# Performance work log

Measured on AMD Instinct MI355X. Metric: run time of the kernel, lower is better.

## Reference

```python
import jax, jax.numpy as jnp
import numpy as np

B, SEQ_LEN, PRED_LEN, LABEL_LEN, PERIOD, N_CH = 32, 2048, 1024, 512, 256, 256
K = SEQ_LEN // PERIOD   # seg_num_x = 8
L = PRED_LEN // PERIOD  # seg_num_y = 4
EPS = 1e-5


def setup_inputs() -> dict:
    key = jax.random.key(0)
    k1, k2, k3, k4, k5, k6, k7 = jax.random.split(key, 7)
    x_enc = jax.random.normal(k1, (B, SEQ_LEN, N_CH), jnp.float32)
    x_mark_enc = jax.random.normal(k2, (B, SEQ_LEN, 4), jnp.float32)
    x_dec = jax.random.normal(k3, (B, LABEL_LEN + PRED_LEN, N_CH), jnp.float32)
    x_mark_dec = jax.random.normal(k4, (B, LABEL_LEN + PRED_LEN, 4), jnp.float32)
    # base_model abstracted as a linear map on the time axis of a [B, PERIOD, N] segment.
    # Scaled ~1/sqrt(P) so repeated powers (up to K+L-1 = 11) stay numerically tame.
    W_base = jax.random.normal(k5, (PERIOD, PERIOD), jnp.float32) * (0.9 / np.sqrt(PERIOD))
    # new_encoders[j]: nn.Linear(seg_num_x, 1) -> weight row [K] + bias scalar per j.
    W_enc = jax.random.normal(k6, (L, K), jnp.float32) * (1.0 / np.sqrt(K))
    b_enc = jax.random.normal(k7, (L,), jnp.float32) * 0.01
    return {"x_enc": x_enc, "x_mark_enc": x_mark_enc, "x_dec": x_dec,
            "x_mark_dec": x_mark_dec, "W_base": W_base, "W_enc": W_enc, "b_enc": b_enc}


def reference(x_enc, x_mark_enc, x_dec, x_mark_dec, W_base, W_enc, b_enc):
    Bv, S, N = x_enc.shape
    # per-series normalization over time (means is .detach()'d in torch; fwd math identical)
    means = jnp.mean(x_enc, axis=1, keepdims=True)                  # [B,1,N]
    xc = x_enc - means
    stdev = jnp.sqrt(jnp.var(xc, axis=1, keepdims=True) + EPS)      # [B,1,N]
    xn = xc / stdev

    # split into K segments of length PERIOD: [K, B, P, N]
    segs = xn.reshape(Bv, K, PERIOD, N).transpose(1, 0, 2, 3)

    # x_res[l][k] = base_model applied (K - k + l) times to segment k.
    # base(x) = einsum('qp,bpn->bqn', W_base, x), so m applications = W_base^m.
    def step(c, _):
        nxt = W_base @ c
        return nxt, nxt
    _, rest = jax.lax.scan(step, W_base, None, length=K + L - 2)
    powers = jnp.concatenate([W_base[None], rest], axis=0)          # powers[i] = W^(i+1)

    exps = (K - jnp.arange(K))[None, :] + jnp.arange(L)[:, None]    # [L,K]
    Wlk = powers[exps - 1]                                          # [L,K,P,P]
    x_res = jnp.einsum('lkqp,kbpn->lkbqn', Wlk, segs)               # [L,K,B,P,N]

    # dec_out_part[l] = sum_k W_enc[l,k] * x_res[l][k] + b_enc[l] * ones
    dec = jnp.einsum('lk,lkbqn->lbqn', W_enc, x_res) + b_enc[:, None, None, None]
    dec = dec.transpose(1, 0, 2, 3).reshape(Bv, L * PERIOD, N)      # cat over time

    # de-normalize
    dec = dec * stdev[:, 0, :][:, None, :] + means[:, 0, :][:, None, :]
    return dec[:, -PRED_LEN:, :]
```

## Files before the change

### kernel.cpp

```cpp
#include <hip/hip_runtime.h>
#include <cstdint>
#include <cstddef>


typedef unsigned short ushort_t;
typedef unsigned int uint_t;
typedef __attribute__((ext_vector_type(8))) short bf16x8;
typedef __attribute__((ext_vector_type(16))) float f32x16;

__device__ __forceinline__ ushort_t f32_to_bf16(float f) {
    uint_t u = __float_as_uint(f);
    u += 0x7FFFu + ((u >> 16) & 1u);
    return (ushort_t)(u >> 16);
}
__device__ __forceinline__ float bf16_to_f32(ushort_t h) {
    return __uint_as_float((uint_t)h << 16);
}

struct PowOps { int sa[4]; int sb[4]; int sd[4]; };

__global__ void powmul(const float* __restrict__ Wb, float* __restrict__ Pw, PowOps ops) {
    __shared__ float As[4 * 256];
    const int mat = blockIdx.x;
    const int r0  = blockIdx.y * 4;
    const int tid = threadIdx.x;
    const float* A  = (ops.sa[mat] < 0) ? Wb : Pw + (size_t)ops.sa[mat] * 65536;
    const float* Bm = (ops.sb[mat] < 0) ? Wb : Pw + (size_t)ops.sb[mat] * 65536;
    float* C        = Pw + (size_t)ops.sd[mat] * 65536;
#pragma unroll
    for (int i = 0; i < 4; ++i) As[i * 256 + tid] = A[(size_t)(r0 + i) * 256 + tid];
    __syncthreads();
    float a0 = 0.f, a1 = 0.f, a2 = 0.f, a3 = 0.f;
    for (int p = 0; p < 256; p += 8) {
        float bv[8];
#pragma unroll
        for (int u = 0; u < 8; ++u) bv[u] = Bm[(size_t)(p + u) * 256 + tid];
#pragma unroll
        for (int u = 0; u < 8; ++u) {
            a0 += As[0 * 256 + p + u] * bv[u];
            a1 += As[1 * 256 + p + u] * bv[u];
            a2 += As[2 * 256 + p + u] * bv[u];
            a3 += As[3 * 256 + p + u] * bv[u];
        }
    }
    C[(size_t)(r0 + 0) * 256 + tid] = a0;
    C[(size_t)(r0 + 1) * 256 + tid] = a1;
    C[(size_t)(r0 + 2) * 256 + tid] = a2;
    C[(size_t)(r0 + 3) * 256 + tid] = a3;
}

__global__ void prepPb(const float* __restrict__ Pw, const float* __restrict__ Wb,
                       ushort_t* __restrict__ Pb, float* __restrict__ prs) {
    const int ib = blockIdx.x;
    const int e  = ib >> 2;
    const int rq = ib & 3;
    const int tid = threadIdx.x;
    const int q  = rq * 64 + (tid >> 2);
    const int cc = tid & 3;
    uint2* dst = (uint2*)(Pb + (size_t)e * 65536 + q * 256 + cc * 64);
    float s = 0.f;
    if (e == 0) {
#pragma unroll
        for (int i = 0; i < 16; ++i) {
            uint2 o; o.x = 0u; o.y = 0u;
            const int col0 = cc * 64 + i * 4;
            if (q >= col0 && q < col0 + 4) {
                const int j = q - col0;
                if (j == 0) o.x = 0x3F80u; else if (j == 1) o.x = 0x3F800000u;
                else if (j == 2) o.y = 0x3F80u; else o.y = 0x3F800000u;
            }
            dst[i] = o;
        }
        s = 1.0f;
    } else {
        const float* src = (e == 1) ? Wb : (Pw + (size_t)(e - 2) * 65536);
        const float4* sp = (const float4*)(src + (size_t)q * 256 + cc * 64);
#pragma unroll
        for (int i = 0; i < 16; ++i) {
            const float4 v = sp[i];
            const ushort_t h0 = f32_to_bf16(v.x), h1 = f32_to_bf16(v.y);
            const ushort_t h2 = f32_to_bf16(v.z), h3 = f32_to_bf16(v.w);
            s += bf16_to_f32(h0) + bf16_to_f32(h1) + bf16_to_f32(h2) + bf16_to_f32(h3);
            uint2 o; o.x = (uint_t)h0 | ((uint_t)h1 << 16); o.y = (uint_t)h2 | ((uint_t)h3 << 16);
            dst[i] = o;
        }
    }
    s += __shfl_xor(s, 1);
    s += __shfl_xor(s, 2);
    if (cc == 0) prs[e * 256 + q] = s;
}

#define GLOAD_LDS16(gsrc, ldst) \
    __builtin_amdgcn_global_load_lds((const __attribute__((address_space(1))) void*)(gsrc), \
                                     (__attribute__((address_space(3))) void*)(ldst), 16, 0, 0)

__global__ __launch_bounds__(512, 4) void gemm_v(
    const ushort_t* __restrict__ Pb, const float* __restrict__ x,
    ushort_t* __restrict__ vt,
    float* __restrict__ psS1, float* __restrict__ psS2)
{
    __shared__ ushort_t sA[2][4096];
    __shared__ ushort_t sB[3][8192];
    __shared__ uint_t   scr[32 * 64];

    const int bid  = blockIdx.x;
    const int k    = bid & 7;
    const int colT = bid >> 3;
    const int e    = 8 - k;

    const int tid  = threadIdx.x;
    const int lane = tid & 63;
    const int w    = tid >> 6;
    const int wm   = w >> 2;
    const int wq   = w & 3;
    const int li   = lane & 31, lg = lane >> 5;
    const int lq3  = (li >> 1) & 3;
    const int lrow = 2 * (lane >> 3) + ((lane >> 2) & 1);
    const int kc   = (lane & 3) ^ ((lane >> 3) & 3);

    const ushort_t* pbb = Pb + (size_t)e * 65536;
    const int b  = colT >> 1;
    const int n0 = (colT & 1) * 128;
    const float* xseg = x + ((size_t)b * 2048 + k * 256) * 256 + n0;

    const int xp = tid >> 5;
    const int xn = (tid & 31) * 4;

    float4 xr[2];
    float s1[4] = {0, 0, 0, 0}, s2[4] = {0, 0, 0, 0};

#define BSTAGE(bf_, kt_) do { \
    const int p0_ = (kt_) * 32 + kc * 8; \
    GLOAD_LDS16(pbb + (w * 32 + 0  + lrow) * 256 + p0_, &sB[bf_][(w * 32 + 0)  * 32]); \
    GLOAD_LDS16(pbb + (w * 32 + 16 + lrow) * 256 + p0_, &sB[bf_][(w * 32 + 16) * 32]); \
} while (0)

#define XLOAD(kt_) do { \
    xr[0] = *(const float4*)(xseg + (size_t)((kt_) * 32 + xp)      * 256 + xn); \
    xr[1] = *(const float4*)(xseg + (size_t)((kt_) * 32 + xp + 16) * 256 + xn); \
} while (0)

#define SCRW() do { \
    _Pragma("unroll") \
    for (int i_ = 0; i_ < 2; ++i_) { \
        const float4 v_ = xr[i_]; \
        s1[0] += v_.x; s2[0] += v_.x * v_.x; \
        s1[1] += v_.y; s2[1] += v_.y * v_.y; \
        s1[2] += v_.z; s2[2] += v_.z * v_.z; \
        s1[3] += v_.w; s2[3] += v_.w * v_.w; \
        uint2 p_; \
        p_.x = (uint_t)f32_to_bf16(v_.x) | ((uint_t)f32_to_bf16(v_.y) << 16); \
        p_.y = (uint_t)f32_to_bf16(v_.z) | ((uint_t)f32_to_bf16(v_.w) << 16); \
        *(uint2*)(scr + (xp + 16 * i_) * 64 + (xn >> 1)) = p_; \
    } \
} while (0)

#define FRAGBUILD(buf_) do { \
    const int R_ = tid >> 2;                  \
    const int pc_ = tid & 3;                  \
    const int sh_ = (R_ & 1) * 16; \
    uint_t o_[4]; \
    _Pragma("unroll") \
    for (int u_ = 0; u_ < 4; ++u_) { \
        const uint_t w0_ = scr[(pc_ * 8 + 2 * u_ + 0) * 64 + (R_ >> 1)]; \
        const uint_t w1_ = scr[(pc_ * 8 + 2 * u_ + 1) * 64 + (R_ >> 1)]; \
        o_[u_] = ((w0_ >> sh_) & 0xFFFFu) | (((w1_ >> sh_) & 0xFFFFu) << 16); \
    } \
    uint4 q_; q_.x = o_[0]; q_.y = o_[1]; q_.z = o_[2]; q_.w = o_[3]; \
    *(uint4*)((char*)&sA[buf_][0] + R_ * 64 + ((pc_ ^ ((R_ >> 1) & 3)) << 4)) = q_; \
} while (0)

    f32x16 acc[2][2];
#pragma unroll
    for (int mm = 0; mm < 2; ++mm)
#pragma unroll
        for (int nn = 0; nn < 2; ++nn)
#pragma unroll
            for (int rr = 0; rr < 16; ++rr) acc[mm][nn][rr] = 0.0f;

    XLOAD(0);
    asm volatile("s_waitcnt vmcnt(0)" ::: "memory");
    SCRW();
    asm volatile("s_waitcnt lgkmcnt(0)" ::: "memory");
    __builtin_amdgcn_s_barrier();
    asm volatile("" ::: "memory");
    FRAGBUILD(0);
    BSTAGE(0, 0);
    asm volatile("" ::: "memory");
    XLOAD(1);
    asm volatile("" ::: "memory");
    BSTAGE(1, 1);
    asm volatile("s_waitcnt lgkmcnt(0)" ::: "memory");

#define VKT(kt_) do { \
    if ((kt_) < 7) { asm volatile("s_waitcnt vmcnt(2)" ::: "memory"); } \
    else           { asm volatile("s_waitcnt vmcnt(0)" ::: "memory"); } \
    __builtin_amdgcn_s_barrier(); \
    asm volatile("" ::: "memory"); \
    const ushort_t* pa_ = &sA[(kt_) & 1][0]; \
    const ushort_t* px_ = &sB[(kt_) % 3][0]; \
    bf16x8 af0, af1, xf0, xf1; \
    { const int sl_ = lg ^ lq3; \
      const int ro_ = (li >> 1) * 64 + (li & 1) * 32 + sl_ * 8; \
      af0 = *(const bf16x8*)(pa_ + wm * 2048 + ro_); \
      af1 = *(const bf16x8*)(pa_ + wm * 2048 + 1024 + ro_); \
      xf0 = *(const bf16x8*)(px_ + wq * 2048 + ro_); \
      xf1 = *(const bf16x8*)(px_ + wq * 2048 + 1024 + ro_); } \
    if ((kt_) < 7) { SCRW(); }    \
    if ((kt_) < 6) { \
        XLOAD((kt_) + 2); \
        asm volatile("" ::: "memory"); \
        BSTAGE(((kt_) + 2) % 3, (kt_) + 2); \
    } \
    __builtin_amdgcn_s_setprio(1); \
    acc[0][0] = __builtin_amdgcn_mfma_f32_32x32x16_bf16(af0, xf0, acc[0][0], 0, 0, 0); \
    acc[0][1] = __builtin_amdgcn_mfma_f32_32x32x16_bf16(af0, xf1, acc[0][1], 0, 0, 0); \
    acc[1][0] = __builtin_amdgcn_mfma_f32_32x32x16_bf16(af1, xf0, acc[1][0], 0, 0, 0); \
    acc[1][1] = __builtin_amdgcn_mfma_f32_32x32x16_bf16(af1, xf1, acc[1][1], 0, 0, 0); \
    { const int sl_ = (2 + lg) ^ lq3; \
      const int ro_ = (li >> 1) * 64 + (li & 1) * 32 + sl_ * 8; \
      af0 = *(const bf16x8*)(pa_ + wm * 2048 + ro_); \
      af1 = *(const bf16x8*)(pa_ + wm * 2048 + 1024 + ro_); \
      xf0 = *(const bf16x8*)(px_ + wq * 2048 + ro_); \
      xf1 = *(const bf16x8*)(px_ + wq * 2048 + 1024 + ro_); } \
    acc[0][0] = __builtin_amdgcn_mfma_f32_32x32x16_bf16(af0, xf0, acc[0][0], 0, 0, 0); \
    acc[0][1] = __builtin_amdgcn_mfma_f32_32x32x16_bf16(af0, xf1, acc[0][1], 0, 0, 0); \
    acc[1][0] = __builtin_amdgcn_mfma_f32_32x32x16_bf16(af1, xf0, acc[1][0], 0, 0, 0); \
    acc[1][1] = __builtin_amdgcn_mfma_f32_32x32x16_bf16(af1, xf1, acc[1][1], 0, 0, 0); \
    __builtin_amdgcn_s_setprio(0); \
    asm volatile("" ::: "memory"); \
    if ((kt_) < 7) { \
        asm volatile("s_waitcnt lgkmcnt(0)" ::: "memory"); \
        __builtin_amdgcn_s_barrier(); \
        asm volatile("" ::: "memory"); \
        FRAGBUILD(((kt_) + 1) & 1); \
        asm volatile("s_waitcnt lgkmcnt(0)" ::: "memory"); \
    } \
} while (0)

    VKT(0); VKT(1); VKT(2); VKT(3); VKT(4); VKT(5); VKT(6); VKT(7);
#undef VKT
#undef FRAGBUILD
#undef SCRW
#undef XLOAD
#undef BSTAGE

    ushort_t* vb = vt + (size_t)k * 2097152;
#pragma unroll
    for (int mm = 0; mm < 2; ++mm)
#pragma unroll
        for (int nn = 0; nn < 2; ++nn) {
            const int q = wq * 64 + nn * 32 + li;
#pragma unroll
            for (int rr = 0; rr < 16; ++rr) {
                const int c = colT * 128 + wm * 64 + mm * 32 + ((rr & 3) + 8 * (rr >> 2) + 4 * lg);
                vb[(size_t)c * 256 + q] = f32_to_bf16(acc[mm][nn][rr]);
            }
        }

    __syncthreads();
    float* sf = (float*)&sB[0][0];
    *(float4*)(sf + xp * 128 + xn)        = make_float4(s1[0], s1[1], s1[2], s1[3]);
    *(float4*)(sf + 2048 + xp * 128 + xn) = make_float4(s2[0], s2[1], s2[2], s2[3]);
    __syncthreads();
    if (tid < 128) {
        float a = 0.f;
#pragma unroll
        for (int r = 0; r < 16; ++r) a += sf[r * 128 + tid];
        psS1[(size_t)k * 8192 + colT * 128 + tid] = a;
    } else if (tid < 256) {
        const int tt = tid - 128;
        float a = 0.f;
#pragma unroll
        for (int r = 0; r < 16; ++r) a += sf[2048 + r * 128 + tt];
        psS2[(size_t)k * 8192 + colT * 128 + tt] = a;
    }
}

__global__ void combine(const ushort_t* __restrict__ vt, const float* __restrict__ Wenc,
                        ushort_t* __restrict__ c,
                        const float* __restrict__ psS1, const float* __restrict__ psS2,
                        const float* __restrict__ prs, const ushort_t* __restrict__ Pb,
                        float* __restrict__ meanv, float* __restrict__ stdv,
                        float* __restrict__ rsA) {
    __shared__ float uf[256];
    const int bid = blockIdx.x;
    const int t   = threadIdx.x;
    if (bid < 1024) {
        const int col = bid * 8 + (t >> 5);
        const size_t off = (size_t)col * 256 + (t & 31) * 8;
        float a0[8] = {0,0,0,0,0,0,0,0}, a1[8] = {0,0,0,0,0,0,0,0};
        float a2[8] = {0,0,0,0,0,0,0,0}, a3[8] = {0,0,0,0,0,0,0,0};
#pragma unroll
        for (int k = 0; k < 8; ++k) {
            const bf16x8 v = *(const bf16x8*)(vt + (size_t)k * 2097152 + off);
            const float w0 = Wenc[0 * 8 + k], w1 = Wenc[1 * 8 + k];
            const float w2 = Wenc[2 * 8 + k], w3 = Wenc[3 * 8 + k];
#pragma unroll
            for (int j = 0; j < 8; ++j) {
                const float f = bf16_to_f32((ushort_t)v[j]);
                a0[j] += w0 * f; a1[j] += w1 * f; a2[j] += w2 * f; a3[j] += w3 * f;
            }
        }
        bf16x8 o0, o1, o2, o3;
#pragma unroll
        for (int j = 0; j < 8; ++j) {
            o0[j] = (short)f32_to_bf16(a0[j]); o1[j] = (short)f32_to_bf16(a1[j]);
            o2[j] = (short)f32_to_bf16(a2[j]); o3[j] = (short)f32_to_bf16(a3[j]);
        }
        *(bf16x8*)(c + 0 * 2097152 + off) = o0;
        *(bf16x8*)(c + 1 * 2097152 + off) = o1;
        *(bf16x8*)(c + 2 * 2097152 + off) = o2;
        *(bf16x8*)(c + 3 * 2097152 + off) = o3;
    } else if (bid < 1056) {
        const int b = bid - 1024;
        const int col = b * 256 + t;
        float s = 0.f, q = 0.f;
#pragma unroll
        for (int k = 0; k < 8; ++k) {
            s += psS1[(size_t)k * 8192 + col];
            q += psS2[(size_t)k * 8192 + col];
        }
        const float mean = s * (1.0f / 2048.0f);
        float var = q * (1.0f / 2048.0f) - mean * mean;
        var = fmaxf(var, 0.0f);
        meanv[col] = mean;
        stdv [col] = sqrtf(var + 1e-5f);
    } else {
        const int l = bid - 1056;
        float u = 0.f;
#pragma unroll
        for (int k = 0; k < 8; ++k) u += Wenc[l * 8 + k] * prs[(8 - k) * 256 + t];
        uf[t] = u;
        __syncthreads();
        const uint2* rp = (const uint2*)(Pb + (size_t)l * 65536 + t * 256);
        float s = 0.f;
#pragma unroll
        for (int i = 0; i < 64; ++i) {
            const uint2 v = rp[i];
            s += bf16_to_f32((ushort_t)(v.x & 0xffff)) * uf[i * 4 + 0]
               + bf16_to_f32((ushort_t)(v.x >> 16))    * uf[i * 4 + 1]
               + bf16_to_f32((ushort_t)(v.y & 0xffff)) * uf[i * 4 + 2]
               + bf16_to_f32((ushort_t)(v.y >> 16))    * uf[i * 4 + 3];
        }
        rsA[l * 256 + t] = s;
    }
}

__global__ __launch_bounds__(256, 2) void gemm2(
    const ushort_t* __restrict__ Pb, const ushort_t* __restrict__ c,
    const float* __restrict__ meanv, const float* __restrict__ stdv,
    const float* __restrict__ rsA, const float* __restrict__ benc,
    float* __restrict__ out)
{
    __shared__ ushort_t sAa[3][4096];
    __shared__ ushort_t sBb[3][4096];

    const int bid  = blockIdx.x;
    const int xcd  = bid & 7;
    const int g    = bid >> 3;
    const int colT = xcd + ((g & 7) << 3);
    const int rest = g >> 3;
    const int l    = rest >> 1;
    const int qpT  = rest & 1;

    const int tid  = threadIdx.x;
    const int lane = tid & 63;
    const int w    = tid >> 6;
    const int wm   = w >> 1, wn = w & 1;
    const int li   = lane & 31, lg = lane >> 5;
    const int lq3  = (li >> 1) & 3;
    const int lrow = 2 * (lane >> 3) + ((lane >> 2) & 1);
    const int kc   = (lane & 3) ^ ((lane >> 3) & 3);

    const ushort_t* ab = Pb + (size_t)l * 65536 + (size_t)(qpT * 128) * 256;
    const ushort_t* cb = c + ((size_t)l * 8192 + colT * 128) * 256;

#define GSTAGE(bf_, kt_) do { \
    const int p0_ = (kt_) * 32 + kc * 8; \
    GLOAD_LDS16(ab + (w * 32 + 0  + lrow) * 256 + p0_, &sAa[bf_][(w * 32 + 0)  * 32]); \
    GLOAD_LDS16(ab + (w * 32 + 16 + lrow) * 256 + p0_, &sAa[bf_][(w * 32 + 16) * 32]); \
    GLOAD_LDS16(cb + (w * 32 + 0  + lrow) * 256 + p0_, &sBb[bf_][(w * 32 + 0)  * 32]); \
    GLOAD_LDS16(cb + (w * 32 + 16 + lrow) * 256 + p0_, &sBb[bf_][(w * 32 + 16) * 32]); \
} while (0)

    f32x16 acc[2][2];
#pragma unroll
    for (int mm = 0; mm < 2; ++mm)
#pragma unroll
        for (int nn = 0; nn < 2; ++nn)
#pragma unroll
            for (int rr = 0; rr < 16; ++rr) acc[mm][nn][rr] = 0.0f;

    GSTAGE(0, 0);
    GSTAGE(1, 1);

#define GKT(kt_) do { \
    if ((kt_) < 7) { asm volatile("s_waitcnt vmcnt(4)" ::: "memory"); } \
    else           { asm volatile("s_waitcnt vmcnt(0)" ::: "memory"); } \
    __builtin_amdgcn_s_barrier(); \
    asm volatile("" ::: "memory"); \
    const ushort_t* pa_ = &sAa[(kt_) % 3][0]; \
    const ushort_t* px_ = &sBb[(kt_) % 3][0]; \
    bf16x8 af[2][2], xf[2][2]; \
    _Pragma("unroll") \
    for (int ks = 0; ks < 2; ++ks) { \
        const int sl = ((ks << 1) + lg) ^ lq3; \
        const int ro = (li >> 1) * 64 + (li & 1) * 32 + sl * 8; \
        af[ks][0] = *(const bf16x8*)(pa_ + wm * 2048 + ro); \
        af[ks][1] = *(const bf16x8*)(pa_ + wm * 2048 + 1024 + ro); \
        xf[ks][0] = *(const bf16x8*)(px_ + wn * 2048 + ro); \
        xf[ks][1] = *(const bf16x8*)(px_ + wn * 2048 + 1024 + ro); \
    } \
    if ((kt_) < 6) { GSTAGE(((kt_) + 2) % 3, (kt_) + 2); } \
    __builtin_amdgcn_s_setprio(1); \
    _Pragma("unroll") \
    for (int ks = 0; ks < 2; ++ks) { \
        acc[0][0] = __builtin_amdgcn_mfma_f32_32x32x16_bf16(af[ks][0], xf[ks][0], acc[0][0], 0, 0, 0); \
        acc[0][1] = __builtin_amdgcn_mfma_f32_32x32x16_bf16(af[ks][0], xf[ks][1], acc[0][1], 0, 0, 0); \
        acc[1][0] = __builtin_amdgcn_mfma_f32_32x32x16_bf16(af[ks][1], xf[ks][0], acc[1][0], 0, 0, 0); \
        acc[1][1] = __builtin_amdgcn_mfma_f32_32x32x16_bf16(af[ks][1], xf[ks][1], acc[1][1], 0, 0, 0); \
    } \
    __builtin_amdgcn_s_setprio(0); \
    asm volatile("" ::: "memory"); \
} while (0)

    GKT(0); GKT(1); GKT(2); GKT(3); GKT(4); GKT(5); GKT(6); GKT(7);
#undef GKT
#undef GSTAGE

    const float be = benc[l];
    float mn[2], sd[2];
#pragma unroll
    for (int nn = 0; nn < 2; ++nn) {
        const int col = colT * 128 + wn * 64 + nn * 32 + li;
        mn[nn] = meanv[col];
        sd[nn] = stdv [col];
    }
#pragma unroll
    for (int mm = 0; mm < 2; ++mm)
#pragma unroll
        for (int nn = 0; nn < 2; ++nn) {
            const int col = colT * 128 + wn * 64 + nn * 32 + li;
            const int bq = col >> 8, nq = col & 255;
            const float ben = be * sd[nn];
#pragma unroll
            for (int rr = 0; rr < 16; ++rr) {
                const int trow = l * 256 + qpT * 128 + wm * 64 + mm * 32
                               + ((rr & 3) + 8 * (rr >> 2) + 4 * lg);
                out[((size_t)bq * 1024 + trow) * 256 + nq] =
                    acc[mm][nn][rr] + mn[nn] * (1.0f - rsA[trow]) + ben;
            }
        }
}

extern "C" void kernel_launch(void* const* d_in, const int* in_sizes, int n_in,
                              void* d_out, int out_size, void* d_ws, size_t ws_size,
                              hipStream_t stream) {
    (void)in_sizes; (void)n_in; (void)out_size; (void)ws_size;
    const float* x_enc  = (const float*)d_in[0];
    const float* W_base = (const float*)d_in[4];
    const float* W_enc  = (const float*)d_in[5];
    const float* b_enc  = (const float*)d_in[6];
    float* out = (float*)d_out;

    char* ws = (char*)d_ws;
    float*    wsP    = (float*)(ws);
    ushort_t* wsPb   = (ushort_t*)(ws + 0x200000);
    float*    wsPrs  = (float*)(ws + 0x340000);
    float*    wsS1   = (float*)(ws + 0x350000);
    float*    wsS2   = (float*)(ws + 0x390000);
    float*    wsMean = (float*)(ws + 0x3D0000);
    float*    wsStd  = (float*)(ws + 0x3E0000);
    float*    wsRsA  = (float*)(ws + 0x3F0000);
    ushort_t* wsVt   = (ushort_t*)(ws + 0x400000);
    ushort_t* wsC    = (ushort_t*)(ws + 0x2400000);

    { PowOps o{{-1, 0, 0, 0}, {-1, 0, 0, 0}, {0, 0, 0, 0}};
      powmul<<<dim3(1, 64), 256, 0, stream>>>(W_base, wsP, o); }
    { PowOps o{{0, 0, 0, 0}, {-1, 0, 0, 0}, {1, 2, 0, 0}};
      powmul<<<dim3(2, 64), 256, 0, stream>>>(W_base, wsP, o); }
    { PowOps o{{2, 2, 2, 2}, {-1, 0, 1, 2}, {3, 4, 5, 6}};
      powmul<<<dim3(4, 64), 256, 0, stream>>>(W_base, wsP, o); }

    prepPb<<<36, 256, 0, stream>>>(wsP, W_base, wsPb, wsPrs);

    gemm_v<<<512, 512, 0, stream>>>(wsPb, x_enc, wsVt, wsS1, wsS2);

    combine<<<1060, 256, 0, stream>>>(wsVt, W_enc, wsC, wsS1, wsS2, wsPrs, wsPb,
                                      wsMean, wsStd, wsRsA);

    gemm2<<<512, 256, 0, stream>>>(wsPb, wsC, wsMean, wsStd, wsRsA, b_enc, out);
}
```

Measured before the change: 102.7 us.

## Restructure gemm_v into two halves with batched x staging and padded transpose

The per-k-step pipeline of gemm_v, which interleaved x loads, bf16 transpose and MFMA, becomes two halves. Each half loads 128 rows of x, transposes them into four A-fragment buffers through a scratch area padded to a stride of 65 to avoid LDS bank conflicts, then runs four MFMA k-steps with only one barrier each. The scratch area now aliases the B staging buffers rather than having its own LDS allocation, while the A buffer grows from two slots to four. The aim is fewer barriers and less interleaving overhead in the MFMA loop, at the cost of serialising global x loads ahead of compute in each half and using more LDS in total.

```diff
diff --git a/kernel.cpp b/kernel.cpp
--- a/kernel.cpp
+++ b/kernel.cpp
@@ -99,9 +99,9 @@
     ushort_t* __restrict__ vt,
     float* __restrict__ psS1, float* __restrict__ psS2)
 {
-    __shared__ ushort_t sA[2][4096];
+    __shared__ ushort_t sA[4][4096];
     __shared__ ushort_t sB[3][8192];
-    __shared__ uint_t   scr[32 * 64];
+    uint_t* scr = (uint_t*)&sB[1][0];
 
     const int bid  = blockIdx.x;
     const int k    = bid & 7;
@@ -126,7 +126,7 @@
     const int xp = tid >> 5;
     const int xn = (tid & 31) * 4;
 
-    float4 xr[2];
+    float4 xr0[4], xr1[4];
     float s1[4] = {0, 0, 0, 0}, s2[4] = {0, 0, 0, 0};
 
 #define BSTAGE(bf_, kt_) do { \
@@ -135,39 +135,44 @@
     GLOAD_LDS16(pbb + (w * 32 + 16 + lrow) * 256 + p0_, &sB[bf_][(w * 32 + 16) * 32]); \
 } while (0)
 
-#define XLOAD(kt_) do { \
-    xr[0] = *(const float4*)(xseg + (size_t)((kt_) * 32 + xp)      * 256 + xn); \
-    xr[1] = *(const float4*)(xseg + (size_t)((kt_) * 32 + xp + 16) * 256 + xn); \
-} while (0)
-
-#define SCRW() do { \
+#define XLOADS(dst_, p0_) do { \
     _Pragma("unroll") \
-    for (int i_ = 0; i_ < 2; ++i_) { \
-        const float4 v_ = xr[i_]; \
+    for (int i_ = 0; i_ < 4; ++i_) \
+        dst_[i_] = *(const float4*)(xseg + (size_t)((p0_) + xp + 16 * i_) * 256 + xn); \
+} while (0)
+
+#define SCRW(src_) do { \
+    _Pragma("unroll") \
+    for (int i_ = 0; i_ < 4; ++i_) { \
+        const float4 v_ = src_[i_]; \
         s1[0] += v_.x; s2[0] += v_.x * v_.x; \
         s1[1] += v_.y; s2[1] += v_.y * v_.y; \
         s1[2] += v_.z; s2[2] += v_.z * v_.z; \
         s1[3] += v_.w; s2[3] += v_.w * v_.w; \
-        uint2 p_; \
-        p_.x = (uint_t)f32_to_bf16(v_.x) | ((uint_t)f32_to_bf16(v_.y) << 16); \
-        p_.y = (uint_t)f32_to_bf16(v_.z) | ((uint_t)f32_to_bf16(v_.w) << 16); \
-        *(uint2*)(scr + (xp + 16 * i_) * 64 + (xn >> 1)) = p_; \
+        const int pl_ = xp + 16 * i_; \
+        scr[pl_ * 65 + (xn >> 1)]     = (uint_t)f32_to_bf16(v_.x) | ((uint_t)f32_to_bf16(v_.y) << 16); \
+        scr[pl_ * 65 + (xn >> 1) + 1] = (uint_t)f32_to_bf16(v_.z) | ((uint_t)f32_to_bf16(v_.w) << 16); \
     } \
 } while (0)
 
-#define FRAGBUILD(buf_) do { \
-    const int R_ = tid >> 2;                  \
-    const int pc_ = tid & 3;                  \
+#define FRAGBUILD(s_) do { \
+    const int R_  = tid >> 2;               \
+    const int pc_ = tid & 3; \
+    const int np_ = R_ >> 1; \
     const int sh_ = (R_ & 1) * 16; \
-    uint_t o_[4]; \
     _Pragma("unroll") \
-    for (int u_ = 0; u_ < 4; ++u_) { \
-        const uint_t w0_ = scr[(pc_ * 8 + 2 * u_ + 0) * 64 + (R_ >> 1)]; \
-        const uint_t w1_ = scr[(pc_ * 8 + 2 * u_ + 1) * 64 + (R_ >> 1)]; \
-        o_[u_] = ((w0_ >> sh_) & 0xFFFFu) | (((w1_ >> sh_) & 0xFFFFu) << 16); \
+    for (int kh_ = 0; kh_ < 2; ++kh_) { \
+        uint_t o_[4]; \
+        _Pragma("unroll") \
+        for (int u_ = 0; u_ < 4; ++u_) { \
+            const int m_ = kh_ * 16 + pc_ * 4 + u_; \
+            const uint_t w0_ = scr[(2 * m_) * 65 + np_]; \
+            const uint_t w1_ = scr[(2 * m_ + 1) * 65 + np_]; \
+            o_[u_] = ((w0_ >> sh_) & 0xFFFFu) | (((w1_ >> sh_) & 0xFFFFu) << 16); \
+        } \
+        uint4 q_; q_.x = o_[0]; q_.y = o_[1]; q_.z = o_[2]; q_.w = o_[3]; \
+        *(uint4*)((char*)&sA[0][0] + (2 * (s_) + kh_) * 8192 + R_ * 64 + ((pc_ ^ ((R_ >> 1) & 3)) << 4)) = q_; \
     } \
-    uint4 q_; q_.x = o_[0]; q_.y = o_[1]; q_.z = o_[2]; q_.w = o_[3]; \
-    *(uint4*)((char*)&sA[buf_][0] + R_ * 64 + ((pc_ ^ ((R_ >> 1) & 3)) << 4)) = q_; \
 } while (0)
 
     f32x16 acc[2][2];
@@ -178,71 +183,78 @@
 #pragma unroll
             for (int rr = 0; rr < 16; ++rr) acc[mm][nn][rr] = 0.0f;
 
-    XLOAD(0);
-    asm volatile("s_waitcnt vmcnt(0)" ::: "memory");
-    SCRW();
-    asm volatile("s_waitcnt lgkmcnt(0)" ::: "memory");
-    __builtin_amdgcn_s_barrier();
-    asm volatile("" ::: "memory");
-    FRAGBUILD(0);
-    BSTAGE(0, 0);
-    asm volatile("" ::: "memory");
-    XLOAD(1);
-    asm volatile("" ::: "memory");
-    BSTAGE(1, 1);
-    asm volatile("s_waitcnt lgkmcnt(0)" ::: "memory");
-
-#define VKT(kt_) do { \
-    if ((kt_) < 7) { asm volatile("s_waitcnt vmcnt(2)" ::: "memory"); } \
-    else           { asm volatile("s_waitcnt vmcnt(0)" ::: "memory"); } \
+#define GKT(i_, kt_, STAGEOP, VM) do { \
+    VM; \
     __builtin_amdgcn_s_barrier(); \
     asm volatile("" ::: "memory"); \
-    const ushort_t* pa_ = &sA[(kt_) & 1][0]; \
-    const ushort_t* px_ = &sB[(kt_) % 3][0]; \
-    bf16x8 af0, af1, xf0, xf1; \
+    const ushort_t* pa_ = &sA[i_][0]; \
+    const ushort_t* px_ = &sB[(i_) % 3][0]; \
+    bf16x8 af0, af1, xf0, xf1, ag0, ag1, xg0, xg1; \
     { const int sl_ = lg ^ lq3; \
       const int ro_ = (li >> 1) * 64 + (li & 1) * 32 + sl_ * 8; \
       af0 = *(const bf16x8*)(pa_ + wm * 2048 + ro_); \
       af1 = *(const bf16x8*)(pa_ + wm * 2048 + 1024 + ro_); \
       xf0 = *(const bf16x8*)(px_ + wq * 2048 + ro_); \
       xf1 = *(const bf16x8*)(px_ + wq * 2048 + 1024 + ro_); } \
-    if ((kt_) < 7) { SCRW(); }    \
-    if ((kt_) < 6) { \
-        XLOAD((kt_) + 2); \
-        asm volatile("" ::: "memory"); \
-        BSTAGE(((kt_) + 2) % 3, (kt_) + 2); \
-    } \
+    { const int sl_ = (2 + lg) ^ lq3; \
+      const int ro_ = (li >> 1) * 64 + (li & 1) * 32 + sl_ * 8; \
+      ag0 = *(const bf16x8*)(pa_ + wm * 2048 + ro_); \
+      ag1 = *(const bf16x8*)(pa_ + wm * 2048 + 1024 + ro_); \
+      xg0 = *(const bf16x8*)(px_ + wq * 2048 + ro_); \
+      xg1 = *(const bf16x8*)(px_ + wq * 2048 + 1024 + ro_); } \
+    STAGEOP; \
     __builtin_amdgcn_s_setprio(1); \
     acc[0][0] = __builtin_amdgcn_mfma_f32_32x32x16_bf16(af0, xf0, acc[0][0], 0, 0, 0); \
     acc[0][1] = __builtin_amdgcn_mfma_f32_32x32x16_bf16(af0, xf1, acc[0][1], 0, 0, 0); \
     acc[1][0] = __builtin_amdgcn_mfma_f32_32x32x16_bf16(af1, xf0, acc[1][0], 0, 0, 0); \
     acc[1][1] = __builtin_amdgcn_mfma_f32_32x32x16_bf16(af1, xf1, acc[1][1], 0, 0, 0); \
-    { const int sl_ = (2 + lg) ^ lq3; \
-      const int ro_ = (li >> 1) * 64 + (li & 1) * 32 + sl_ * 8; \
-      af0 = *(const bf16x8*)(pa_ + wm * 2048 + ro_); \
-      af1 = *(const bf16x8*)(pa_ + wm * 2048 + 1024 + ro_); \
-      xf0 = *(const bf16x8*)(px_ + wq * 2048 + ro_); \
-      xf1 = *(const bf16x8*)(px_ + wq * 2048 + 1024 + ro_); } \
-    acc[0][0] = __builtin_amdgcn_mfma_f32_32x32x16_bf16(af0, xf0, acc[0][0], 0, 0, 0); \
-    acc[0][1] = __builtin_amdgcn_mfma_f32_32x32x16_bf16(af0, xf1, acc[0][1], 0, 0, 0); \
-    acc[1][0] = __builtin_amdgcn_mfma_f32_32x32x16_bf16(af1, xf0, acc[1][0], 0, 0, 0); \
-    acc[1][1] = __builtin_amdgcn_mfma_f32_32x32x16_bf16(af1, xf1, acc[1][1], 0, 0, 0); \
+    acc[0][0] = __builtin_amdgcn_mfma_f32_32x32x16_bf16(ag0, xg0, acc[0][0], 0, 0, 0); \
+    acc[0][1] = __builtin_amdgcn_mfma_f32_32x32x16_bf16(ag0, xg1, acc[0][1], 0, 0, 0); \
+    acc[1][0] = __builtin_amdgcn_mfma_f32_32x32x16_bf16(ag1, xg0, acc[1][0], 0, 0, 0); \
+    acc[1][1] = __builtin_amdgcn_mfma_f32_32x32x16_bf16(ag1, xg1, acc[1][1], 0, 0, 0); \
     __builtin_amdgcn_s_setprio(0); \
     asm volatile("" ::: "memory"); \
-    if ((kt_) < 7) { \
-        asm volatile("s_waitcnt lgkmcnt(0)" ::: "memory"); \
-        __builtin_amdgcn_s_barrier(); \
-        asm volatile("" ::: "memory"); \
-        FRAGBUILD(((kt_) + 1) & 1); \
-        asm volatile("s_waitcnt lgkmcnt(0)" ::: "memory"); \
-    } \
-} while (0)
-
-    VKT(0); VKT(1); VKT(2); VKT(3); VKT(4); VKT(5); VKT(6); VKT(7);
-#undef VKT
+} while (0)
+
+#define VMW(n_) asm volatile("s_waitcnt vmcnt(" #n_ ")" ::: "memory")
+#define LGW()   asm volatile("s_waitcnt lgkmcnt(0)" ::: "memory")
+#define BARM()  do { __builtin_amdgcn_s_barrier(); asm volatile("" ::: "memory"); } while (0)
+
+#define HALF(h_) do { \
+    XLOADS(xr0, (h_) * 128);         \
+    XLOADS(xr1, (h_) * 128 + 64);    \
+    VMW(4);                           \
+    SCRW(xr0); \
+    LGW(); \
+    BARM(); \
+    FRAGBUILD(0); \
+    BSTAGE(0, (h_) * 4);              \
+    LGW(); \
+    BARM(); \
+    VMW(2);                           \
+    SCRW(xr1); \
+    LGW(); \
+    BARM(); \
+    FRAGBUILD(1); \
+    LGW();                            \
+    BARM();                           \
+    BSTAGE(1, (h_) * 4 + 1); \
+    GKT(0, (h_) * 4 + 0, BSTAGE(2, (h_) * 4 + 2), VMW(2)); \
+    GKT(1, (h_) * 4 + 1, BSTAGE(0, (h_) * 4 + 3), VMW(2)); \
+    GKT(2, (h_) * 4 + 2, , VMW(2)); \
+    GKT(3, (h_) * 4 + 3, , VMW(0)); \
+} while (0)
+
+    HALF(0);
+    HALF(1);
+#undef HALF
+#undef GKT
+#undef VMW
+#undef LGW
+#undef BARM
 #undef FRAGBUILD
 #undef SCRW
-#undef XLOAD
+#undef XLOADS
 #undef BSTAGE
 
     ushort_t* vb = vt + (size_t)k * 2097152;
```

Measured after the change: 145.2 us. 1.41x slower.
